# Optimization experiments

Measured on AMD Instinct MI355X. Metric: run time of the kernel, lower is better.

Reference implementation:

```python
import jax, jax.numpy as jnp
import numpy as np

N_NODES = 100000
N_EDGES = 1600000
IN_FEATS = 64
OUT_FEATS = 64
DIM = 3
N_KERNELS = 4


def setup_inputs() -> dict:
    key = jax.random.key(0)
    ks = jax.random.split(key, 8)
    feat = jax.random.normal(ks[0], (N_NODES, IN_FEATS), dtype=jnp.float32)
    pseudo = jax.random.uniform(ks[1], (N_EDGES, DIM), dtype=jnp.float32)
    src = jax.random.randint(ks[2], (N_EDGES,), 0, N_NODES, dtype=jnp.int32)
    dst = jax.random.randint(ks[3], (N_EDGES,), 0, N_NODES, dtype=jnp.int32)
    W_fc = jax.random.normal(ks[4], (N_KERNELS * OUT_FEATS, IN_FEATS), dtype=jnp.float32) * 0.1
    mu = jax.random.normal(ks[5], (N_KERNELS, DIM), dtype=jnp.float32)
    inv_sigma = jax.random.uniform(ks[6], (N_KERNELS, DIM), dtype=jnp.float32) + 0.5
    bias = jnp.zeros((OUT_FEATS,), dtype=jnp.float32)
    return {"feat": feat, "pseudo": pseudo, "src": src, "dst": dst,
            "W_fc": W_fc, "mu": mu, "inv_sigma": inv_sigma, "bias": bias}


def reference(feat, pseudo, src, dst, W_fc, mu, inv_sigma, bias):
    N = feat.shape[0]
    K, out = N_KERNELS, OUT_FEATS
    # node projections: [N, K, out]
    h = (feat @ W_fc.T).reshape(N, K, out)
    # per-edge Gaussian kernel weights: [E, K]
    diff = pseudo[:, None, :] - mu[None, :, :]            # [E, K, dim]
    g = jnp.exp(jnp.sum(-0.5 * diff * diff * (inv_sigma[None] ** 2), axis=-1))
    # sum-aggregate: sum_k sum_{e: dst=v} h[src_e, k] * g[e, k]
    # (kernel sum and edge sum commute for sum reducer; loop over K avoids [E,K,out])
    rst = jnp.zeros((N, out), dtype=feat.dtype)
    for k in range(K):
        msg = h[:, k, :][src] * g[:, k:k + 1]             # [E, out]
        rst = rst + jax.ops.segment_sum(msg, dst, num_segments=N)
    # residual (Identity since in_feats == out_feats) + bias
    rst = rst + feat + bias
    return rst
```

## Files before the change

kernel.cpp:

```cpp
#include <hip/hip_runtime.h>

#define N_NODES_C 100000
#define N_EDGES_C 1600000
#define IN_F 64
#define OUT_F 64
#define NK 4
#define SCAN_BLK 256
#define NBLK ((N_NODES_C + SCAN_BLK - 1) / SCAN_BLK)
#define EBLK (N_EDGES_C / 256)
#define CPAD 16
#define NSLICE 8
#define SLICE_N (N_NODES_C / NSLICE)
#define SCAT_GRID 2048

__device__ __forceinline__ unsigned int f2bf(float x) {
    unsigned int u = __float_as_uint(x);
    return (u + 0x7fffu + ((u >> 16) & 1u)) >> 16;
}
__device__ __forceinline__ float bflo(unsigned int u) { return __uint_as_float(u << 16); }
__device__ __forceinline__ float bfhi(unsigned int u) { return __uint_as_float(u & 0xffff0000u); }

__global__ __launch_bounds__(256) void hist_gauss_kernel(
    const int* __restrict__ dst, const float* __restrict__ pseudo,
    const float* __restrict__ mu, const float* __restrict__ inv_sigma,
    int* __restrict__ cnt, uint2* __restrict__ g8)
{
    const int e = blockIdx.x * 256 + threadIdx.x;
    if (e >= N_EDGES_C) return;
    atomicAdd(&cnt[dst[e]], 1);
    const float p0 = pseudo[(size_t)e * 3 + 0];
    const float p1 = pseudo[(size_t)e * 3 + 1];
    const float p2 = pseudo[(size_t)e * 3 + 2];
    float g[NK];
    #pragma unroll
    for (int k = 0; k < NK; ++k) {
        const float d0 = p0 - mu[k*3+0], d1 = p1 - mu[k*3+1], d2 = p2 - mu[k*3+2];
        const float s0 = inv_sigma[k*3+0], s1 = inv_sigma[k*3+1], s2 = inv_sigma[k*3+2];
        const float ex = -0.5f * (d0*d0*s0*s0 + d1*d1*s1*s1 + d2*d2*s2*s2);
        g[k] = __expf(ex);
    }
    uint2 r;
    r.x = f2bf(g[0]) | (f2bf(g[1]) << 16);
    r.y = f2bf(g[2]) | (f2bf(g[3]) << 16);
    g8[e] = r;
}

__global__ __launch_bounds__(256, 2) void proj_kernel(
    const float* __restrict__ feat, const float* __restrict__ W,
    unsigned short* __restrict__ hb, int n_nodes)
{
    __shared__ float frow[2][IN_F];
    const int t = threadIdx.x;
    const int o = t >> 2;
    const int k = t & 3;
    float wreg[IN_F];
    {
        const float4* W4 = reinterpret_cast<const float4*>(W + (size_t)(k * OUT_F + o) * IN_F);
        #pragma unroll
        for (int i = 0; i < IN_F / 4; ++i) {
            float4 v = W4[i];
            wreg[4*i+0] = v.x; wreg[4*i+1] = v.y; wreg[4*i+2] = v.z; wreg[4*i+3] = v.w;
        }
    }
    const int nn2 = n_nodes >> 1;
    for (int q = blockIdx.x; q < nn2; q += gridDim.x) {
        const int n0 = q << 1;
        if (t < 32) {
            float4 v = reinterpret_cast<const float4*>(feat + (size_t)n0 * IN_F)[t];
            const int r = t >> 4, c = (t & 15) * 4;
            frow[r][c+0] = v.x; frow[r][c+1] = v.y; frow[r][c+2] = v.z; frow[r][c+3] = v.w;
        }
        __syncthreads();
        float a0 = 0.f, b0 = 0.f, a1 = 0.f, b1 = 0.f;
        #pragma unroll
        for (int i = 0; i < IN_F; i += 2) {
            a0 = fmaf(frow[0][i],   wreg[i],   a0);
            b0 = fmaf(frow[0][i+1], wreg[i+1], b0);
            a1 = fmaf(frow[1][i],   wreg[i],   a1);
            b1 = fmaf(frow[1][i+1], wreg[i+1], b1);
        }
        hb[(size_t)n0 * 256 + t]       = (unsigned short)f2bf(a0 + b0);
        hb[(size_t)(n0 + 1) * 256 + t] = (unsigned short)f2bf(a1 + b1);
        __syncthreads();
    }
}

__global__ __launch_bounds__(256) void scan1_kernel(
    const int* __restrict__ cnt, int* __restrict__ bsum)
{
    __shared__ int s[SCAN_BLK];
    int i = blockIdx.x * SCAN_BLK + threadIdx.x;
    int v = (i < N_NODES_C) ? cnt[i] : 0;
    s[threadIdx.x] = v; __syncthreads();
    for (int off = SCAN_BLK / 2; off > 0; off >>= 1) {
        if (threadIdx.x < off) s[threadIdx.x] += s[threadIdx.x + off];
        __syncthreads();
    }
    if (threadIdx.x == 0) bsum[blockIdx.x] = s[0];
}

__global__ __launch_bounds__(256) void scan23_kernel(
    const int* __restrict__ cnt, const int* __restrict__ bsum,
    int* __restrict__ row_start, int* __restrict__ cursor_pad)
{
    __shared__ int pre[SCAN_BLK];
    __shared__ int s[SCAN_BLK];
    const int t = threadIdx.x;
    int p = 0;
    for (int i = t; i < (int)blockIdx.x; i += SCAN_BLK) p += bsum[i];
    pre[t] = p; __syncthreads();
    for (int off = SCAN_BLK / 2; off > 0; off >>= 1) {
        if (t < off) pre[t] += pre[t + off];
        __syncthreads();
    }
    const int boff = pre[0];
    const int i = blockIdx.x * SCAN_BLK + t;
    int v = (i < N_NODES_C) ? cnt[i] : 0;
    s[t] = v; __syncthreads();
    for (int off = 1; off < SCAN_BLK; off <<= 1) {
        int x = (t >= off) ? s[t - off] : 0;
        __syncthreads();
        s[t] += x;
        __syncthreads();
    }
    if (i < N_NODES_C) {
        int ex = s[t] - v + boff;
        row_start[i] = ex;
        cursor_pad[(size_t)i * CPAD] = ex;
        if (i == N_NODES_C - 1) row_start[N_NODES_C] = ex + v;
    }
}

__global__ __launch_bounds__(256) void scatter_kernel(
    const int* __restrict__ src, const int* __restrict__ dst,
    const uint2* __restrict__ g8, int* __restrict__ cursor_pad,
    uint4* __restrict__ rec)
{
    const int slice = (int)blockIdx.x & 7;
    const int w     = (int)blockIdx.x >> 3;
    const int lo = slice * SLICE_N, hi = lo + SLICE_N;
    for (int c = w; c < EBLK; c += SCAT_GRID / NSLICE) {
        const int e = c * 256 + (int)threadIdx.x;
        const int d = dst[e];
        if (d >= lo && d < hi) {
            const int s = src[e];
            const uint2 g = g8[e];
            const int pos = atomicAdd(&cursor_pad[(size_t)d * CPAD], 1);
            uint4 r; r.x = (unsigned int)s; r.y = g.x; r.z = g.y; r.w = 0u;
            rec[pos] = r;
        }
    }
}

__global__ __launch_bounds__(256, 2) void gather_kernel(
    const int* __restrict__ row_start, const uint4* __restrict__ rec,
    const unsigned short* __restrict__ hb,
    const float* __restrict__ feat, const float* __restrict__ bias,
    float* __restrict__ out, int n_nodes)
{
    const int lane = threadIdx.x & 63;
    const int v = (blockIdx.x * 256 + threadIdx.x) >> 6;
    if (v >= n_nodes) return;
    const int r0 = row_start[v];
    const int r1 = row_start[v + 1];
    float acc = 0.f;
    int j = r0;
    const int jend4 = r0 + ((r1 - r0) & ~3);
    if (j < jend4) {
        uint4 a0 = rec[j+0], a1 = rec[j+1], a2 = rec[j+2], a3 = rec[j+3];
        j += 4;
        for (; j < jend4; j += 4) {
            const uint2 h0 = *(const uint2*)(hb + (size_t)a0.x * 256 + lane * 4);
            const uint2 h1 = *(const uint2*)(hb + (size_t)a1.x * 256 + lane * 4);
            const uint2 h2 = *(const uint2*)(hb + (size_t)a2.x * 256 + lane * 4);
            const uint2 h3 = *(const uint2*)(hb + (size_t)a3.x * 256 + lane * 4);
            const uint4 b0 = rec[j+0], b1 = rec[j+1], b2 = rec[j+2], b3 = rec[j+3];
            acc += bflo(a0.y)*bflo(h0.x) + bfhi(a0.y)*bfhi(h0.x)
                 + bflo(a0.z)*bflo(h0.y) + bfhi(a0.z)*bfhi(h0.y);
            acc += bflo(a1.y)*bflo(h1.x) + bfhi(a1.y)*bfhi(h1.x)
                 + bflo(a1.z)*bflo(h1.y) + bfhi(a1.z)*bfhi(h1.y);
            acc += bflo(a2.y)*bflo(h2.x) + bfhi(a2.y)*bfhi(h2.x)
                 + bflo(a2.z)*bflo(h2.y) + bfhi(a2.z)*bfhi(h2.y);
            acc += bflo(a3.y)*bflo(h3.x) + bfhi(a3.y)*bfhi(h3.x)
                 + bflo(a3.z)*bflo(h3.y) + bfhi(a3.z)*bfhi(h3.y);
            a0 = b0; a1 = b1; a2 = b2; a3 = b3;
        }
        {
            const uint2 h0 = *(const uint2*)(hb + (size_t)a0.x * 256 + lane * 4);
            const uint2 h1 = *(const uint2*)(hb + (size_t)a1.x * 256 + lane * 4);
            const uint2 h2 = *(const uint2*)(hb + (size_t)a2.x * 256 + lane * 4);
            const uint2 h3 = *(const uint2*)(hb + (size_t)a3.x * 256 + lane * 4);
            acc += bflo(a0.y)*bflo(h0.x) + bfhi(a0.y)*bfhi(h0.x)
                 + bflo(a0.z)*bflo(h0.y) + bfhi(a0.z)*bfhi(h0.y);
            acc += bflo(a1.y)*bflo(h1.x) + bfhi(a1.y)*bfhi(h1.x)
                 + bflo(a1.z)*bflo(h1.y) + bfhi(a1.z)*bfhi(h1.y);
            acc += bflo(a2.y)*bflo(h2.x) + bfhi(a2.y)*bfhi(h2.x)
                 + bflo(a2.z)*bflo(h2.y) + bfhi(a2.z)*bfhi(h2.y);
            acc += bflo(a3.y)*bflo(h3.x) + bfhi(a3.y)*bfhi(h3.x)
                 + bflo(a3.z)*bflo(h3.y) + bfhi(a3.z)*bfhi(h3.y);
        }
    }
    for (; j < r1; ++j) {
        const uint4 ra = rec[j];
        const uint2 ha = *(const uint2*)(hb + (size_t)ra.x * 256 + lane * 4);
        acc += bflo(ra.y)*bflo(ha.x) + bfhi(ra.y)*bfhi(ha.x)
             + bflo(ra.z)*bflo(ha.y) + bfhi(ra.z)*bfhi(ha.y);
    }
    out[(size_t)v * OUT_F + lane] = acc + feat[(size_t)v * OUT_F + lane] + bias[lane];
}

extern "C" void kernel_launch(void* const* d_in, const int* in_sizes, int n_in,
                              void* d_out, int out_size, void* d_ws, size_t ws_size,
                              hipStream_t stream) {
    const float* feat      = (const float*)d_in[0];
    const float* pseudo    = (const float*)d_in[1];
    const int*   src       = (const int*)d_in[2];
    const int*   dst       = (const int*)d_in[3];
    const float* W_fc      = (const float*)d_in[4];
    const float* mu        = (const float*)d_in[5];
    const float* inv_sigma = (const float*)d_in[6];
    const float* bias      = (const float*)d_in[7];
    float* out = (float*)d_out;

    char* ws = (char*)d_ws;
    unsigned short* hb = (unsigned short*)ws;  ws += (size_t)N_NODES_C * 256 * 2;
    uint2* g8          = (uint2*)ws;           ws += (size_t)N_EDGES_C * 8;
    uint4* rec         = (uint4*)ws;           ws += (size_t)N_EDGES_C * 16;
    int* cursor_pad    = (int*)ws;             ws += (size_t)N_NODES_C * CPAD * 4;
    int* cnt           = (int*)ws;             ws += (size_t)N_NODES_C * 4;
    int* row_start     = (int*)ws;             ws += (size_t)(N_NODES_C + 4) * 4;
    int* bsum          = (int*)ws;             ws += 512 * 4;

    hipMemsetAsync(cnt, 0, (size_t)N_NODES_C * 4, stream);
    hist_gauss_kernel<<<EBLK, 256, 0, stream>>>(dst, pseudo, mu, inv_sigma, cnt, g8);
    proj_kernel<<<2048, 256, 0, stream>>>(feat, W_fc, hb, N_NODES_C);
    scan1_kernel<<<NBLK, SCAN_BLK, 0, stream>>>(cnt, bsum);
    scan23_kernel<<<NBLK, SCAN_BLK, 0, stream>>>(cnt, bsum, row_start, cursor_pad);
    scatter_kernel<<<SCAT_GRID, 256, 0, stream>>>(src, dst, g8, cursor_pad, rec);
    gather_kernel<<<(N_NODES_C * 64 + 255) / 256, 256, 0, stream>>>(
        row_start, rec, hb, feat, bias, out, N_NODES_C);
}
```

Baseline: 349.5 us.

## Fuse Gaussian weights into scatter, slice histogram atomics, widen projection to four nodes

Moves the per-edge Gaussian kernel computation out of the histogram pass and into the scatter pass. This removes the intermediate g8 buffer write and re-read. The histogram now uses the same dst-sliced grid as scatter, so each block's atomics fall in one node range for better cache locality. It re-reads dst eight times across slices. The projection kernel processes four nodes per iteration with float4 shared-memory reads, giving more weight reuse per loaded row.

```diff
diff --git a/kernel.cpp b/kernel.cpp
--- a/kernel.cpp
+++ b/kernel.cpp
@@ -20,36 +20,23 @@
 __device__ __forceinline__ float bflo(unsigned int u) { return __uint_as_float(u << 16); }
 __device__ __forceinline__ float bfhi(unsigned int u) { return __uint_as_float(u & 0xffff0000u); }
 
-__global__ __launch_bounds__(256) void hist_gauss_kernel(
-    const int* __restrict__ dst, const float* __restrict__ pseudo,
-    const float* __restrict__ mu, const float* __restrict__ inv_sigma,
-    int* __restrict__ cnt, uint2* __restrict__ g8)
-{
-    const int e = blockIdx.x * 256 + threadIdx.x;
-    if (e >= N_EDGES_C) return;
-    atomicAdd(&cnt[dst[e]], 1);
-    const float p0 = pseudo[(size_t)e * 3 + 0];
-    const float p1 = pseudo[(size_t)e * 3 + 1];
-    const float p2 = pseudo[(size_t)e * 3 + 2];
-    float g[NK];
-    #pragma unroll
-    for (int k = 0; k < NK; ++k) {
-        const float d0 = p0 - mu[k*3+0], d1 = p1 - mu[k*3+1], d2 = p2 - mu[k*3+2];
-        const float s0 = inv_sigma[k*3+0], s1 = inv_sigma[k*3+1], s2 = inv_sigma[k*3+2];
-        const float ex = -0.5f * (d0*d0*s0*s0 + d1*d1*s1*s1 + d2*d2*s2*s2);
-        g[k] = __expf(ex);
-    }
-    uint2 r;
-    r.x = f2bf(g[0]) | (f2bf(g[1]) << 16);
-    r.y = f2bf(g[2]) | (f2bf(g[3]) << 16);
-    g8[e] = r;
+__global__ __launch_bounds__(256) void hist_kernel(
+    const int* __restrict__ dst, int* __restrict__ cnt)
+{
+    const int slice = (int)blockIdx.x & 7;
+    const int w     = (int)blockIdx.x >> 3;
+    const int lo = slice * SLICE_N, hi = lo + SLICE_N;
+    for (int c = w; c < EBLK; c += SCAT_GRID / NSLICE) {
+        const int d = dst[c * 256 + (int)threadIdx.x];
+        if (d >= lo && d < hi) atomicAdd(&cnt[d], 1);
+    }
 }
 
 __global__ __launch_bounds__(256, 2) void proj_kernel(
     const float* __restrict__ feat, const float* __restrict__ W,
     unsigned short* __restrict__ hb, int n_nodes)
 {
-    __shared__ float frow[2][IN_F];
+    __shared__ float frow[4][IN_F];
     const int t = threadIdx.x;
     const int o = t >> 2;
     const int k = t & 3;
@@ -62,25 +49,32 @@
             wreg[4*i+0] = v.x; wreg[4*i+1] = v.y; wreg[4*i+2] = v.z; wreg[4*i+3] = v.w;
         }
     }
-    const int nn2 = n_nodes >> 1;
-    for (int q = blockIdx.x; q < nn2; q += gridDim.x) {
-        const int n0 = q << 1;
-        if (t < 32) {
+    const int nn4 = n_nodes >> 2;
+    for (int q = blockIdx.x; q < nn4; q += gridDim.x) {
+        const int n0 = q << 2;
+        if (t < 64) {
             float4 v = reinterpret_cast<const float4*>(feat + (size_t)n0 * IN_F)[t];
-            const int r = t >> 4, c = (t & 15) * 4;
-            frow[r][c+0] = v.x; frow[r][c+1] = v.y; frow[r][c+2] = v.z; frow[r][c+3] = v.w;
-        }
-        __syncthreads();
-        float a0 = 0.f, b0 = 0.f, a1 = 0.f, b1 = 0.f;
+            reinterpret_cast<float4*>(frow[t >> 4])[t & 15] = v;
+        }
+        __syncthreads();
+        const float4* f0 = reinterpret_cast<const float4*>(frow[0]);
+        const float4* f1 = reinterpret_cast<const float4*>(frow[1]);
+        const float4* f2 = reinterpret_cast<const float4*>(frow[2]);
+        const float4* f3 = reinterpret_cast<const float4*>(frow[3]);
+        float a0 = 0.f, a1 = 0.f, a2 = 0.f, a3 = 0.f;
         #pragma unroll
-        for (int i = 0; i < IN_F; i += 2) {
-            a0 = fmaf(frow[0][i],   wreg[i],   a0);
-            b0 = fmaf(frow[0][i+1], wreg[i+1], b0);
-            a1 = fmaf(frow[1][i],   wreg[i],   a1);
-            b1 = fmaf(frow[1][i+1], wreg[i+1], b1);
-        }
-        hb[(size_t)n0 * 256 + t]       = (unsigned short)f2bf(a0 + b0);
-        hb[(size_t)(n0 + 1) * 256 + t] = (unsigned short)f2bf(a1 + b1);
+        for (int i = 0; i < IN_F / 4; ++i) {
+            const float4 v0 = f0[i], v1 = f1[i], v2 = f2[i], v3 = f3[i];
+            const float w0 = wreg[4*i], w1 = wreg[4*i+1], w2 = wreg[4*i+2], w3 = wreg[4*i+3];
+            a0 = fmaf(v0.x,w0, fmaf(v0.y,w1, fmaf(v0.z,w2, fmaf(v0.w,w3, a0))));
+            a1 = fmaf(v1.x,w0, fmaf(v1.y,w1, fmaf(v1.z,w2, fmaf(v1.w,w3, a1))));
+            a2 = fmaf(v2.x,w0, fmaf(v2.y,w1, fmaf(v2.z,w2, fmaf(v2.w,w3, a2))));
+            a3 = fmaf(v3.x,w0, fmaf(v3.y,w1, fmaf(v3.z,w2, fmaf(v3.w,w3, a3))));
+        }
+        hb[(size_t)(n0+0) * 256 + t] = (unsigned short)f2bf(a0);
+        hb[(size_t)(n0+1) * 256 + t] = (unsigned short)f2bf(a1);
+        hb[(size_t)(n0+2) * 256 + t] = (unsigned short)f2bf(a2);
+        hb[(size_t)(n0+3) * 256 + t] = (unsigned short)f2bf(a3);
         __syncthreads();
     }
 }
@@ -133,9 +127,13 @@
 
 __global__ __launch_bounds__(256) void scatter_kernel(
     const int* __restrict__ src, const int* __restrict__ dst,
-    const uint2* __restrict__ g8, int* __restrict__ cursor_pad,
+    const float* __restrict__ pseudo, const float* __restrict__ mu,
+    const float* __restrict__ inv_sigma, int* __restrict__ cursor_pad,
     uint4* __restrict__ rec)
 {
+    float mm[NK*3], ss[NK*3];
+    #pragma unroll
+    for (int i = 0; i < NK*3; ++i) { mm[i] = mu[i]; ss[i] = inv_sigma[i]; }
     const int slice = (int)blockIdx.x & 7;
     const int w     = (int)blockIdx.x >> 3;
     const int lo = slice * SLICE_N, hi = lo + SLICE_N;
@@ -143,10 +141,22 @@
         const int e = c * 256 + (int)threadIdx.x;
         const int d = dst[e];
         if (d >= lo && d < hi) {
-            const int s = src[e];
-            const uint2 g = g8[e];
+            const float p0 = pseudo[(size_t)e * 3 + 0];
+            const float p1 = pseudo[(size_t)e * 3 + 1];
+            const float p2 = pseudo[(size_t)e * 3 + 2];
+            float g[NK];
+            #pragma unroll
+            for (int k = 0; k < NK; ++k) {
+                const float d0 = p0 - mm[k*3+0], d1 = p1 - mm[k*3+1], d2 = p2 - mm[k*3+2];
+                const float s0 = ss[k*3+0], s1 = ss[k*3+1], s2 = ss[k*3+2];
+                g[k] = __expf(-0.5f * (d0*d0*s0*s0 + d1*d1*s1*s1 + d2*d2*s2*s2));
+            }
             const int pos = atomicAdd(&cursor_pad[(size_t)d * CPAD], 1);
-            uint4 r; r.x = (unsigned int)s; r.y = g.x; r.z = g.y; r.w = 0u;
+            uint4 r;
+            r.x = (unsigned int)src[e];
+            r.y = f2bf(g[0]) | (f2bf(g[1]) << 16);
+            r.z = f2bf(g[2]) | (f2bf(g[3]) << 16);
+            r.w = 0u;
             rec[pos] = r;
         }
     }
@@ -224,7 +234,6 @@
 
     char* ws = (char*)d_ws;
     unsigned short* hb = (unsigned short*)ws;  ws += (size_t)N_NODES_C * 256 * 2;
-    uint2* g8          = (uint2*)ws;           ws += (size_t)N_EDGES_C * 8;
     uint4* rec         = (uint4*)ws;           ws += (size_t)N_EDGES_C * 16;
     int* cursor_pad    = (int*)ws;             ws += (size_t)N_NODES_C * CPAD * 4;
     int* cnt           = (int*)ws;             ws += (size_t)N_NODES_C * 4;
@@ -232,11 +241,12 @@
     int* bsum          = (int*)ws;             ws += 512 * 4;
 
     hipMemsetAsync(cnt, 0, (size_t)N_NODES_C * 4, stream);
-    hist_gauss_kernel<<<EBLK, 256, 0, stream>>>(dst, pseudo, mu, inv_sigma, cnt, g8);
+    hist_kernel<<<SCAT_GRID, 256, 0, stream>>>(dst, cnt);
     proj_kernel<<<2048, 256, 0, stream>>>(feat, W_fc, hb, N_NODES_C);
     scan1_kernel<<<NBLK, SCAN_BLK, 0, stream>>>(cnt, bsum);
     scan23_kernel<<<NBLK, SCAN_BLK, 0, stream>>>(cnt, bsum, row_start, cursor_pad);
-    scatter_kernel<<<SCAT_GRID, 256, 0, stream>>>(src, dst, g8, cursor_pad, rec);
+    scatter_kernel<<<SCAT_GRID, 256, 0, stream>>>(src, dst, pseudo, mu, inv_sigma,
+                                                  cursor_pad, rec);
     gather_kernel<<<(N_NODES_C * 64 + 255) / 256, 256, 0, stream>>>(
         row_start, rec, hb, feat, bias, out, N_NODES_C);
 }
```

After: 345.7 us. No clear change (-1.1%).
